# Performance work log

Hardware: AMD Instinct MI355X
Metric: run time of the kernel (lower is better)

Reference implementation:

```python
import jax, jax.numpy as jnp
import numpy as np

H, C, G = 4, 32, 64          # heads, per-head channels, num graphs
D_IN, HID = 128, 128          # input feature dim, dueling MLP hidden
NEG_SLOPE = 0.2               # GATv2Conv default negative_slope


def setup_inputs() -> dict:
    key = jax.random.key(0)
    ks = jax.random.split(key, 16)
    N, E = 50000, 800000
    x = jax.random.normal(ks[0], (N, D_IN), jnp.float32)
    edge_index = jax.random.randint(ks[1], (2, E), 0, N, dtype=jnp.int64)
    batch = jnp.sort(jax.random.randint(ks[2], (N,), 0, G, dtype=jnp.int64))
    s_in = 1.0 / np.sqrt(D_IN)
    s_g = 1.0 / np.sqrt(H * C)
    s_h = 1.0 / np.sqrt(HID)
    return {
        "x": x,
        "W_l": jax.random.normal(ks[3], (D_IN, H * C), jnp.float32) * s_in,
        "b_l": jnp.zeros((H * C,), jnp.float32),
        "W_r": jax.random.normal(ks[4], (D_IN, H * C), jnp.float32) * s_in,
        "b_r": jnp.zeros((H * C,), jnp.float32),
        "att": jax.random.normal(ks[5], (H, C), jnp.float32) * (1.0 / np.sqrt(C)),
        "bias": jnp.zeros((H * C,), jnp.float32),
        "Wq1": jax.random.normal(ks[6], (H * C, HID), jnp.float32) * s_g,
        "bq1": jnp.zeros((HID,), jnp.float32),
        "Wq2": jax.random.normal(ks[7], (HID, 2), jnp.float32) * s_h,
        "bq2": jnp.zeros((2,), jnp.float32),
        "Wv1": jax.random.normal(ks[8], (H * C, HID), jnp.float32) * s_g,
        "bv1": jnp.zeros((HID,), jnp.float32),
        "Wv2": jax.random.normal(ks[9], (HID, 1), jnp.float32) * s_h,
        "bv2": jnp.zeros((1,), jnp.float32),
        "edge_index": edge_index,
        "batch": batch,
    }


def reference(x, W_l, b_l, W_r, b_r, att, bias,
              Wq1, bq1, Wq2, bq2, Wv1, bv1, Wv2, bv2,
              edge_index, batch):
    N = x.shape[0]
    # add self loops (PyG GATv2Conv default)
    loop = jnp.arange(N, dtype=edge_index.dtype)
    src = jnp.concatenate([edge_index[0], loop])  # message source j
    dst = jnp.concatenate([edge_index[1], loop])  # aggregation target i

    xl = (x @ W_l + b_l).reshape(N, H, C)  # source transform
    xr = (x @ W_r + b_r).reshape(N, H, C)  # target transform

    # per-edge GATv2 score: a^T LeakyReLU(xl_j + xr_i), shape [Et, H]
    m = jax.nn.leaky_relu(xl[src] + xr[dst], NEG_SLOPE)
    e = jnp.einsum('ehc,hc->eh', m, att)

    # segment softmax over incoming edges of each target node
    emax = jax.ops.segment_max(e, dst, num_segments=N)
    ee = jnp.exp(e - emax[dst])
    denom = jax.ops.segment_sum(ee, dst, num_segments=N)
    alpha = ee / (denom[dst] + 1e-16)  # [Et, H]

    # scatter-add weighted source features, concat heads
    out = jax.ops.segment_sum(alpha[:, :, None] * xl[src], dst, num_segments=N)
    h = jax.nn.relu(out.reshape(N, H * C) + bias)

    # global max pool per graph
    g = jax.ops.segment_max(h, batch, num_segments=G)  # [G, H*C]

    # dueling heads
    q = jax.nn.relu(g @ Wq1 + bq1) @ Wq2 + bq2  # [G, 2]
    v = jax.nn.relu(g @ Wv1 + bv1) @ Wv2 + bv2  # [G, 1]
    return q - q.mean(axis=1, keepdims=True) + v
```

## Files before the change

### kernel.cpp

```cpp
#include <hip/hip_runtime.h>
#include <hip/hip_fp16.h>

#define F   128
#define DIN 128
#define HID 128
#define NEG 0.2f
#define L2E 1.4426950408889634f
#define KNODE 8
#define CAP  64
#define BW   64
#define EPB  2048
#define NBP  800
#define PB   128

typedef _Float16 hvec2 __attribute__((ext_vector_type(2)));
typedef _Float16 half8 __attribute__((ext_vector_type(8)));
typedef float f32x4 __attribute__((ext_vector_type(4)));
union U2 { unsigned u; hvec2 v; };
union UH { _Float16 f; unsigned short u; };

template<int CTRL>
__device__ __forceinline__ float dpp_addf(float x){
    int t = __builtin_amdgcn_update_dpp(0, __float_as_int(x), CTRL, 0xF, 0xF, true);
    return x + __int_as_float(t);
}

__global__ __launch_bounds__(256) void k_fuseA(
        const float* __restrict__ Wl, const float* __restrict__ Wr,
        const float* __restrict__ att,
        const float* __restrict__ bl, const float* __restrict__ br,
        unsigned short* __restrict__ WT, unsigned* __restrict__ att_h,
        float* __restrict__ bcat, unsigned* __restrict__ g_bits, int GF,
        const int* __restrict__ ei, unsigned* __restrict__ table, int E){
    __shared__ unsigned h[NBP];
    if ((int)blockIdx.x < PB){
        const int e = blockIdx.x * 256 + threadIdx.x;
        if (e < 32768){
            const int k = e >> 8, col = e & 255;
            const float w = (col < 128) ? Wl[k * 128 + col] : Wr[k * 128 + (col - 128)];
            UH u; u.f = (_Float16)w;
            WT[col * 128 + k] = u.u;
        }
        if (e < 64){
            float2 a2 = ((const float2*)att)[e];
            U2 r; r.v = hvec2{(_Float16)(a2.x * L2E), (_Float16)(a2.y * L2E)};
            att_h[e] = r.u;
        }
        if (e < 256) bcat[e] = (e < 128) ? bl[e] : br[e - 128];
        if (e < GF) g_bits[e] = 0u;
        return;
    }
    const int blk = (int)blockIdx.x - PB;
    const int t = threadIdx.x;
    for (int b = t; b < NBP; b += 256) h[b] = 0u;
    __syncthreads();
    const int e0 = blk * EPB;
    const int e1 = (e0 + EPB < E) ? e0 + EPB : E;
    for (int e = e0 + t; e < e1; e += 256)
        atomicAdd(&h[ei[E + e] >> 6], 1u);
    __syncthreads();
    unsigned* row = table + (size_t)blk * NBP;
    for (int b = t; b < NBP; b += 256) row[b] = h[b];
}

__global__ __launch_bounds__(512) void k_scanA(unsigned* __restrict__ table,
                        unsigned* __restrict__ btot, int B){
    __shared__ unsigned lds[512];
    const int bin = blockIdx.x;
    const int t = threadIdx.x;
    unsigned v = (t < B) ? table[(size_t)t * NBP + bin] : 0u;
    lds[t] = v; __syncthreads();
    unsigned acc = v;
    for (int off = 1; off < 512; off <<= 1){
        const unsigned add = (t >= off) ? lds[t - off] : 0u; __syncthreads();
        acc += add; lds[t] = acc; __syncthreads();
    }
    if (t < B) table[(size_t)t * NBP + bin] = acc - v;
    if (t == B - 1) btot[bin] = acc;
}

__global__ __launch_bounds__(1024) void k_scanB(const unsigned* __restrict__ btot,
                        unsigned* __restrict__ bbase, int NBK){
    __shared__ unsigned lds[1024];
    const int t = threadIdx.x;
    unsigned v = (t < NBK) ? btot[t] : 0u;
    lds[t] = v; __syncthreads();
    unsigned acc = v;
    for (int off = 1; off < 1024; off <<= 1){
        const unsigned add = (t >= off) ? lds[t - off] : 0u; __syncthreads();
        acc += add; lds[t] = acc; __syncthreads();
    }
    if (t < 1024 && t < NBP) bbase[t] = (t < NBK) ? acc - v : 0u;
}

__global__ __launch_bounds__(256) void k_eplace(const int* __restrict__ ei,
                        const unsigned* __restrict__ table, const unsigned* __restrict__ bbase,
                        unsigned* __restrict__ bucket, int E){
    __shared__ unsigned curs[NBP];
    const int t = threadIdx.x;
    const unsigned* row = table + (size_t)blockIdx.x * NBP;
    for (int b = t; b < NBP; b += 256) curs[b] = row[b] + bbase[b];
    __syncthreads();
    const int e0 = blockIdx.x * EPB;
    const int e1 = (e0 + EPB < E) ? e0 + EPB : E;
    for (int e = e0 + t; e < e1; e += 256){
        const int src = ei[e];
        const int dst = ei[E + e];
        const unsigned pos = atomicAdd(&curs[dst >> 6], 1u);
        bucket[pos] = ((unsigned)src << 6) | (unsigned)(dst & 63);
    }
}

__global__ __launch_bounds__(256) void k_fuseB(
        const unsigned* __restrict__ bbase, const unsigned* __restrict__ btot,
        const unsigned* __restrict__ bucket, unsigned* __restrict__ cnt,
        int* __restrict__ slots, int N, int NBK,
        const float* __restrict__ x, const unsigned short* __restrict__ WT,
        const float* __restrict__ bcat,
        unsigned short* __restrict__ xl_s, unsigned short* __restrict__ xr_s){
    __shared__ unsigned lc[BW];
    if ((int)blockIdx.x < NBK){
        const int b = blockIdx.x;
        const int t = threadIdx.x;
        if (t < BW) lc[t] = 0u;
        __syncthreads();
        const int base = b << 6;
        const unsigned s0 = bbase[b];
        const int n = (int)btot[b];
        for (int e = t; e < n; e += 256){
            const unsigned w = bucket[s0 + e];
            const int d = (int)(w & 63u);
            const unsigned pos = atomicAdd(&lc[d], 1u);
            if (pos < CAP - 1) slots[((size_t)(base + d) << 6) + 1 + pos] = (int)(w >> 6);
        }
        __syncthreads();
        if (t < BW && base + t < N) cnt[base + t] = lc[t];
        return;
    }
    const int mb = (int)blockIdx.x - NBK;
    const int t = threadIdx.x;
    const int w = t >> 6, lane = t & 63;
    const int li = lane & 15, hi = lane >> 4;
    const int rowA = mb * 64 + w * 16 + li;
    const int rA = (rowA < N) ? rowA : N - 1;
    f32x4 acc[16];
    #pragma unroll
    for (int c = 0; c < 16; ++c) acc[c] = f32x4{0.f, 0.f, 0.f, 0.f};
    #pragma unroll
    for (int kt = 0; kt < 4; ++kt){
        const int k0 = kt * 32 + hi * 8;
        const float4 f0 = *(const float4*)(x + (size_t)rA * DIN + k0);
        const float4 f1 = *(const float4*)(x + (size_t)rA * DIN + k0 + 4);
        half8 b;
        b[0] = (_Float16)f0.x; b[1] = (_Float16)f0.y; b[2] = (_Float16)f0.z; b[3] = (_Float16)f0.w;
        b[4] = (_Float16)f1.x; b[5] = (_Float16)f1.y; b[6] = (_Float16)f1.z; b[7] = (_Float16)f1.w;
        #pragma unroll
        for (int c = 0; c < 16; ++c){
            const half8 a = *(const half8*)(WT + (size_t)(c * 16 + li) * 128 + k0);
            acc[c] = __builtin_amdgcn_mfma_f32_16x16x32_f16(a, b, acc[c], 0, 0, 0);
        }
    }
    if (rowA < N){
        #pragma unroll
        for (int c = 0; c < 16; ++c){
            const int col0 = c * 16 + hi * 4;
            const float4 bv = *(const float4*)(bcat + col0);
            UH p0, p1, p2, p3;
            p0.f = (_Float16)(acc[c][0] + bv.x);
            p1.f = (_Float16)(acc[c][1] + bv.y);
            p2.f = (_Float16)(acc[c][2] + bv.z);
            p3.f = (_Float16)(acc[c][3] + bv.w);
            uint2 val;
            val.x = (unsigned)p0.u | ((unsigned)p1.u << 16);
            val.y = (unsigned)p2.u | ((unsigned)p3.u << 16);
            if (col0 < 128) *(uint2*)(xl_s + (size_t)rowA * F + col0)         = val;
            else            *(uint2*)(xr_s + (size_t)rowA * F + (col0 - 128)) = val;
        }
    }
}

__global__ void k_node(const unsigned* __restrict__ xl_h, const unsigned* __restrict__ xr_h,
                       const int* __restrict__ slots, const unsigned* __restrict__ cnt,
                       const unsigned* __restrict__ att_h, const float* __restrict__ bias,
                       const int* __restrict__ batch, unsigned* __restrict__ g_bits, int N){
    const int wid  = (int)(((long long)blockIdx.x * blockDim.x + threadIdx.x) >> 6);
    const int lane = threadIdx.x & 63;
    const int i0 = wid * KNODE;
    if (i0 >= N) return;
    U2 atv; atv.u = att_h[lane];
    const float2 bz = ((const float2*)bias)[lane];
    const hvec2 neg2 = {(_Float16)NEG, (_Float16)NEG};
    float pool0 = 0.f, pool1 = 0.f;
    int curg = __builtin_amdgcn_readfirstlane(batch[i0]);
    const int iend = (i0 + KNODE < N) ? i0 + KNODE : N;

    for (int i = i0; i < iend; ++i){
        const int g = __builtin_amdgcn_readfirstlane(batch[i]);
        if (g != curg){
            atomicMax(&g_bits[curg * F + 2 * lane],     __float_as_uint(pool0));
            atomicMax(&g_bits[curg * F + 2 * lane + 1], __float_as_uint(pool1));
            pool0 = 0.f; pool1 = 0.f; curg = g;
        }
        const int rs = i << 6;
        int dt = (int)cnt[i] + 1;
        if (dt > CAP) dt = CAP;
        U2 xrv; xrv.u = xr_h[(size_t)i * 64 + lane];

        float d0=0.f,d1=0.f,d2=0.f,d3=0.f,d4=0.f,d5=0.f,d6=0.f,d7=0.f;
        float ax0=0.f,ax1=0.f,ax2=0.f,ax3=0.f,ax4=0.f,ax5=0.f,ax6=0.f,ax7=0.f;
        float ay0=0.f,ay1=0.f,ay2=0.f,ay3=0.f,ay4=0.f,ay5=0.f,ay6=0.f,ay7=0.f;

        auto proc = [&](unsigned hv, float& d_, float& ax_, float& ay_){
            U2 xlv; xlv.u = hv;
            hvec2 z = xlv.v + xrv.v;
            hvec2 r = __builtin_elementwise_max(z, z * neg2);
#if __has_builtin(__builtin_amdgcn_fdot2)
            float s = __builtin_amdgcn_fdot2(r, atv.v, 0.f, false);
#else
            float s = fmaf((float)r.x, (float)atv.v.x, (float)r.y * (float)atv.v.y);
#endif
            s = dpp_addf<0xB1>(s);
            s = dpp_addf<0x4E>(s);
            s = dpp_addf<0x124>(s);
            s = dpp_addf<0x128>(s);
            const float p = exp2f(s);
            d_ += p;
            ax_ = fmaf(p, (float)xlv.v.x, ax_);
            ay_ = fmaf(p, (float)xlv.v.y, ay_);
        };

        const int my_src = (lane > 0 && lane < dt) ? slots[rs + lane] : i;
        int e = 0;
        for (; e + 7 < dt; e += 8){
            const int s0 = __builtin_amdgcn_readlane(my_src, e);
            const int s1 = __builtin_amdgcn_readlane(my_src, e + 1);
            const int s2 = __builtin_amdgcn_readlane(my_src, e + 2);
            const int s3 = __builtin_amdgcn_readlane(my_src, e + 3);
            const int s4 = __builtin_amdgcn_readlane(my_src, e + 4);
            const int s5 = __builtin_amdgcn_readlane(my_src, e + 5);
            const int s6 = __builtin_amdgcn_readlane(my_src, e + 6);
            const int s7 = __builtin_amdgcn_readlane(my_src, e + 7);
            const unsigned h0 = xl_h[(size_t)s0 * 64 + lane];
            const unsigned h1 = xl_h[(size_t)s1 * 64 + lane];
            const unsigned h2 = xl_h[(size_t)s2 * 64 + lane];
            const unsigned h3 = xl_h[(size_t)s3 * 64 + lane];
            const unsigned h4 = xl_h[(size_t)s4 * 64 + lane];
            const unsigned h5 = xl_h[(size_t)s5 * 64 + lane];
            const unsigned h6 = xl_h[(size_t)s6 * 64 + lane];
            const unsigned h7 = xl_h[(size_t)s7 * 64 + lane];
            proc(h0, d0, ax0, ay0); proc(h1, d1, ax1, ay1);
            proc(h2, d2, ax2, ay2); proc(h3, d3, ax3, ay3);
            proc(h4, d4, ax4, ay4); proc(h5, d5, ax5, ay5);
            proc(h6, d6, ax6, ay6); proc(h7, d7, ax7, ay7);
        }
        for (; e + 3 < dt; e += 4){
            const int s0 = __builtin_amdgcn_readlane(my_src, e);
            const int s1 = __builtin_amdgcn_readlane(my_src, e + 1);
            const int s2 = __builtin_amdgcn_readlane(my_src, e + 2);
            const int s3 = __builtin_amdgcn_readlane(my_src, e + 3);
            const unsigned h0 = xl_h[(size_t)s0 * 64 + lane];
            const unsigned h1 = xl_h[(size_t)s1 * 64 + lane];
            const unsigned h2 = xl_h[(size_t)s2 * 64 + lane];
            const unsigned h3 = xl_h[(size_t)s3 * 64 + lane];
            proc(h0, d0, ax0, ay0); proc(h1, d1, ax1, ay1);
            proc(h2, d2, ax2, ay2); proc(h3, d3, ax3, ay3);
        }
        for (; e < dt; ++e){
            const int s0 = __builtin_amdgcn_readlane(my_src, e);
            proc(xl_h[(size_t)s0 * 64 + lane], d0, ax0, ay0);
        }

        const float dsum = ((d0 + d1) + (d2 + d3)) + ((d4 + d5) + (d6 + d7));
        const float ax = ((ax0 + ax1) + (ax2 + ax3)) + ((ax4 + ax5) + (ax6 + ax7));
        const float ay = ((ay0 + ay1) + (ay2 + ay3)) + ((ay4 + ay5) + (ay6 + ay7));
        const float inv = 1.f / (dsum + 1e-16f);
        pool0 = fmaxf(pool0, fmaxf(fmaf(ax, inv, bz.x), 0.f));
        pool1 = fmaxf(pool1, fmaxf(fmaf(ay, inv, bz.y), 0.f));
    }
    atomicMax(&g_bits[curg * F + 2 * lane],     __float_as_uint(pool0));
    atomicMax(&g_bits[curg * F + 2 * lane + 1], __float_as_uint(pool1));
}

__global__ void k_dueling(const float* __restrict__ g,
                          const float* __restrict__ Wq1, const float* __restrict__ bq1,
                          const float* __restrict__ Wq2, const float* __restrict__ bq2,
                          const float* __restrict__ Wv1, const float* __restrict__ bv1,
                          const float* __restrict__ Wv2, const float* __restrict__ bv2,
                          float* __restrict__ out){
    __shared__ float gs[F], red0[128], red1[128], red2[128];
    const int t = threadIdx.x, gi = blockIdx.x;
    gs[t] = g[gi * F + t];
    __syncthreads();
    float aq = bq1[t], av = bv1[t];
    for (int k = 0; k < F; ++k){
        aq = fmaf(gs[k], Wq1[k * HID + t], aq);
        av = fmaf(gs[k], Wv1[k * HID + t], av);
    }
    aq = aq > 0.f ? aq : 0.f;
    av = av > 0.f ? av : 0.f;
    red0[t] = aq * Wq2[t * 2 + 0];
    red1[t] = aq * Wq2[t * 2 + 1];
    red2[t] = av * Wv2[t];
    __syncthreads();
    for (int off = 64; off > 0; off >>= 1){
        if (t < off){ red0[t] += red0[t + off]; red1[t] += red1[t + off]; red2[t] += red2[t + off]; }
        __syncthreads();
    }
    if (t == 0){
        const float q0 = red0[0] + bq2[0];
        const float q1 = red1[0] + bq2[1];
        const float v  = red2[0] + bv2[0];
        out[gi * 2 + 0] = 0.5f * (q0 - q1) + v;
        out[gi * 2 + 1] = 0.5f * (q1 - q0) + v;
    }
}

extern "C" void kernel_launch(void* const* d_in, const int* in_sizes, int n_in,
                              void* d_out, int out_size, void* d_ws, size_t ws_size,
                              hipStream_t stream) {
    const float* x    = (const float*)d_in[0];
    const float* Wl   = (const float*)d_in[1];
    const float* bl   = (const float*)d_in[2];
    const float* Wr   = (const float*)d_in[3];
    const float* br   = (const float*)d_in[4];
    const float* att  = (const float*)d_in[5];
    const float* bias = (const float*)d_in[6];
    const float* Wq1  = (const float*)d_in[7];
    const float* bq1  = (const float*)d_in[8];
    const float* Wq2  = (const float*)d_in[9];
    const float* bq2  = (const float*)d_in[10];
    const float* Wv1  = (const float*)d_in[11];
    const float* bv1  = (const float*)d_in[12];
    const float* Wv2  = (const float*)d_in[13];
    const float* bv2  = (const float*)d_in[14];
    const int*   ei   = (const int*)d_in[15];
    const int*   batch= (const int*)d_in[16];
    float* out = (float*)d_out;

    const int N  = in_sizes[0] / DIN;
    const int E  = in_sizes[15] / 2;
    const int Gg = out_size / 2;
    const int GF = Gg * F;
    const int NBK = (N + BW - 1) / BW;
    const int B   = (E + EPB - 1) / EPB;
    const int MMB = (N + 63) / 64;

    unsigned* xl_h   = (unsigned*)d_ws;
    unsigned* xr_h   = xl_h + (size_t)N * 64;
    unsigned* att_h  = xr_h + (size_t)N * 64;
    unsigned* WT     = att_h + 64;
    float*    bcat   = (float*)(WT + 16384);
    unsigned* g_bits = (unsigned*)(bcat + 256);
    unsigned* cnt    = g_bits + GF;
    unsigned* bbase  = cnt + N;
    unsigned* btot   = bbase + NBP;
    unsigned* table  = btot + NBP;
    unsigned* bucket = table + (size_t)B * NBP;
    int*      slots  = (int*)(bucket + E);

    k_fuseA<<<PB + B, 256, 0, stream>>>(Wl, Wr, att, bl, br, (unsigned short*)WT,
                                        att_h, bcat, g_bits, GF, ei, table, E);
    k_scanA<<<NBK, 512, 0, stream>>>(table, btot, B);
    k_scanB<<<1, 1024, 0, stream>>>(btot, bbase, NBK);
    k_eplace<<<B, 256, 0, stream>>>(ei, table, bbase, bucket, E);
    k_fuseB<<<NBK + MMB, 256, 0, stream>>>(bbase, btot, bucket, cnt, slots, N, NBK,
                                           x, (const unsigned short*)WT, bcat,
                                           (unsigned short*)xl_h, (unsigned short*)xr_h);
    {
        const long long waves = (N + KNODE - 1) / KNODE;
        const long long thr = waves * 64;
        k_node<<<(unsigned)((thr + 255) / 256), 256, 0, stream>>>(
            xl_h, xr_h, slots, cnt, att_h, bias, batch, g_bits, N);
    }
    k_dueling<<<Gg, 128, 0, stream>>>((const float*)g_bits, Wq1, bq1, Wq2, bq2,
                                      Wv1, bv1, Wv2, bv2, out);
}
```

Baseline: 144.8 us.

## Process two edges per wavefront step using half-waves with 4 channels per lane

The node kernel now splits each 64-lane wavefront into two 32-lane halves. Each half handles a different incoming edge, and each lane loads 4 fp16 channels (uint2) instead of 2. The per-head score reduction uses two DPP steps plus a ds_swizzle xor-4 in place of four DPP row ops. The halves are combined with a shfl_xor at the end, and only the first half does the pool atomics. This aims to halve the serial edge iterations and issue wider gathers, at the cost of shuffles for source indices, an extra cross-half reduction, and masking of odd tails.

Measured after the change: 157.4 us. +8.7%, slower.

```diff
diff --git a/kernel.cpp b/kernel.cpp
--- a/kernel.cpp
+++ b/kernel.cpp
@@ -22,6 +22,10 @@
 template<int CTRL>
 __device__ __forceinline__ float dpp_addf(float x){
     int t = __builtin_amdgcn_update_dpp(0, __float_as_int(x), CTRL, 0xF, 0xF, true);
+    return x + __int_as_float(t);
+}
+__device__ __forceinline__ float swz_xor4(float x){
+    int t = __builtin_amdgcn_ds_swizzle(__float_as_int(x), 0x101F);
     return x + __int_as_float(t);
 }
 
@@ -185,100 +189,104 @@
                        const int* __restrict__ batch, unsigned* __restrict__ g_bits, int N){
     const int wid  = (int)(((long long)blockIdx.x * blockDim.x + threadIdx.x) >> 6);
     const int lane = threadIdx.x & 63;
+    const int half = lane >> 5;
+    const int cl   = lane & 31;
     const int i0 = wid * KNODE;
     if (i0 >= N) return;
-    U2 atv; atv.u = att_h[lane];
-    const float2 bz = ((const float2*)bias)[lane];
+    const uint2 at2 = ((const uint2*)att_h)[cl];
+    U2 at0, at1; at0.u = at2.x; at1.u = at2.y;
+    const float4 bz = ((const float4*)bias)[cl];
     const hvec2 neg2 = {(_Float16)NEG, (_Float16)NEG};
-    float pool0 = 0.f, pool1 = 0.f;
+    float pool0 = 0.f, pool1 = 0.f, pool2 = 0.f, pool3 = 0.f;
     int curg = __builtin_amdgcn_readfirstlane(batch[i0]);
     const int iend = (i0 + KNODE < N) ? i0 + KNODE : N;
+    const uint2* xl2 = (const uint2*)xl_h;
 
     for (int i = i0; i < iend; ++i){
         const int g = __builtin_amdgcn_readfirstlane(batch[i]);
         if (g != curg){
-            atomicMax(&g_bits[curg * F + 2 * lane],     __float_as_uint(pool0));
-            atomicMax(&g_bits[curg * F + 2 * lane + 1], __float_as_uint(pool1));
-            pool0 = 0.f; pool1 = 0.f; curg = g;
+            if (half == 0){
+                unsigned* gb = &g_bits[curg * F + 4 * cl];
+                atomicMax(&gb[0], __float_as_uint(pool0));
+                atomicMax(&gb[1], __float_as_uint(pool1));
+                atomicMax(&gb[2], __float_as_uint(pool2));
+                atomicMax(&gb[3], __float_as_uint(pool3));
+            }
+            pool0 = pool1 = pool2 = pool3 = 0.f; curg = g;
         }
         const int rs = i << 6;
         int dt = (int)cnt[i] + 1;
         if (dt > CAP) dt = CAP;
-        U2 xrv; xrv.u = xr_h[(size_t)i * 64 + lane];
-
-        float d0=0.f,d1=0.f,d2=0.f,d3=0.f,d4=0.f,d5=0.f,d6=0.f,d7=0.f;
-        float ax0=0.f,ax1=0.f,ax2=0.f,ax3=0.f,ax4=0.f,ax5=0.f,ax6=0.f,ax7=0.f;
-        float ay0=0.f,ay1=0.f,ay2=0.f,ay3=0.f,ay4=0.f,ay5=0.f,ay6=0.f,ay7=0.f;
-
-        auto proc = [&](unsigned hv, float& d_, float& ax_, float& ay_){
-            U2 xlv; xlv.u = hv;
-            hvec2 z = xlv.v + xrv.v;
-            hvec2 r = __builtin_elementwise_max(z, z * neg2);
+        const uint2 xr2 = ((const uint2*)xr_h)[(size_t)i * 32 + cl];
+        U2 xr0, xr1; xr0.u = xr2.x; xr1.u = xr2.y;
+
+        float d0=0.f,d1=0.f,d2=0.f,d3=0.f;
+        float a00=0.f,a01=0.f,a02=0.f,a03=0.f;
+        float a10=0.f,a11=0.f,a12=0.f,a13=0.f;
+        float a20=0.f,a21=0.f,a22=0.f,a23=0.f;
+        float a30=0.f,a31=0.f,a32=0.f,a33=0.f;
+
+        const int my_src = (lane > 0 && lane < dt) ? slots[rs + lane] : i;
+
+        auto proc2 = [&](int e, float& d_, float& x0, float& x1, float& x2, float& x3){
+            const int srcv = __shfl(my_src, e + half, 64);
+            const uint2 xlv = xl2[(size_t)srcv * 32 + cl];
+            U2 b0, b1; b0.u = xlv.x; b1.u = xlv.y;
+            hvec2 z0 = b0.v + xr0.v;
+            hvec2 z1 = b1.v + xr1.v;
+            hvec2 r0 = __builtin_elementwise_max(z0, z0 * neg2);
+            hvec2 r1 = __builtin_elementwise_max(z1, z1 * neg2);
 #if __has_builtin(__builtin_amdgcn_fdot2)
-            float s = __builtin_amdgcn_fdot2(r, atv.v, 0.f, false);
+            float s = __builtin_amdgcn_fdot2(r0, at0.v, 0.f, false);
+            s = __builtin_amdgcn_fdot2(r1, at1.v, s, false);
 #else
-            float s = fmaf((float)r.x, (float)atv.v.x, (float)r.y * (float)atv.v.y);
+            float s = (float)r0.x * (float)at0.v.x + (float)r0.y * (float)at0.v.y
+                    + (float)r1.x * (float)at1.v.x + (float)r1.y * (float)at1.v.y;
 #endif
             s = dpp_addf<0xB1>(s);
             s = dpp_addf<0x4E>(s);
-            s = dpp_addf<0x124>(s);
-            s = dpp_addf<0x128>(s);
-            const float p = exp2f(s);
+            s = swz_xor4(s);
+            const float p = (e + half < dt) ? exp2f(s) : 0.f;
             d_ += p;
-            ax_ = fmaf(p, (float)xlv.v.x, ax_);
-            ay_ = fmaf(p, (float)xlv.v.y, ay_);
+            x0 = fmaf(p, (float)b0.v.x, x0);
+            x1 = fmaf(p, (float)b0.v.y, x1);
+            x2 = fmaf(p, (float)b1.v.x, x2);
+            x3 = fmaf(p, (float)b1.v.y, x3);
         };
 
-        const int my_src = (lane > 0 && lane < dt) ? slots[rs + lane] : i;
         int e = 0;
         for (; e + 7 < dt; e += 8){
-            const int s0 = __builtin_amdgcn_readlane(my_src, e);
-            const int s1 = __builtin_amdgcn_readlane(my_src, e + 1);
-            const int s2 = __builtin_amdgcn_readlane(my_src, e + 2);
-            const int s3 = __builtin_amdgcn_readlane(my_src, e + 3);
-            const int s4 = __builtin_amdgcn_readlane(my_src, e + 4);
-            const int s5 = __builtin_amdgcn_readlane(my_src, e + 5);
-            const int s6 = __builtin_amdgcn_readlane(my_src, e + 6);
-            const int s7 = __builtin_amdgcn_readlane(my_src, e + 7);
-            const unsigned h0 = xl_h[(size_t)s0 * 64 + lane];
-            const unsigned h1 = xl_h[(size_t)s1 * 64 + lane];
-            const unsigned h2 = xl_h[(size_t)s2 * 64 + lane];
-            const unsigned h3 = xl_h[(size_t)s3 * 64 + lane];
-            const unsigned h4 = xl_h[(size_t)s4 * 64 + lane];
-            const unsigned h5 = xl_h[(size_t)s5 * 64 + lane];
-            const unsigned h6 = xl_h[(size_t)s6 * 64 + lane];
-            const unsigned h7 = xl_h[(size_t)s7 * 64 + lane];
-            proc(h0, d0, ax0, ay0); proc(h1, d1, ax1, ay1);
-            proc(h2, d2, ax2, ay2); proc(h3, d3, ax3, ay3);
-            proc(h4, d4, ax4, ay4); proc(h5, d5, ax5, ay5);
-            proc(h6, d6, ax6, ay6); proc(h7, d7, ax7, ay7);
-        }
-        for (; e + 3 < dt; e += 4){
-            const int s0 = __builtin_amdgcn_readlane(my_src, e);
-            const int s1 = __builtin_amdgcn_readlane(my_src, e + 1);
-            const int s2 = __builtin_amdgcn_readlane(my_src, e + 2);
-            const int s3 = __builtin_amdgcn_readlane(my_src, e + 3);
-            const unsigned h0 = xl_h[(size_t)s0 * 64 + lane];
-            const unsigned h1 = xl_h[(size_t)s1 * 64 + lane];
-            const unsigned h2 = xl_h[(size_t)s2 * 64 + lane];
-            const unsigned h3 = xl_h[(size_t)s3 * 64 + lane];
-            proc(h0, d0, ax0, ay0); proc(h1, d1, ax1, ay1);
-            proc(h2, d2, ax2, ay2); proc(h3, d3, ax3, ay3);
-        }
-        for (; e < dt; ++e){
-            const int s0 = __builtin_amdgcn_readlane(my_src, e);
-            proc(xl_h[(size_t)s0 * 64 + lane], d0, ax0, ay0);
-        }
-
-        const float dsum = ((d0 + d1) + (d2 + d3)) + ((d4 + d5) + (d6 + d7));
-        const float ax = ((ax0 + ax1) + (ax2 + ax3)) + ((ax4 + ax5) + (ax6 + ax7));
-        const float ay = ((ay0 + ay1) + (ay2 + ay3)) + ((ay4 + ay5) + (ay6 + ay7));
-        const float inv = 1.f / (dsum + 1e-16f);
-        pool0 = fmaxf(pool0, fmaxf(fmaf(ax, inv, bz.x), 0.f));
-        pool1 = fmaxf(pool1, fmaxf(fmaf(ay, inv, bz.y), 0.f));
-    }
-    atomicMax(&g_bits[curg * F + 2 * lane],     __float_as_uint(pool0));
-    atomicMax(&g_bits[curg * F + 2 * lane + 1], __float_as_uint(pool1));
+            proc2(e,     d0, a00, a01, a02, a03);
+            proc2(e + 2, d1, a10, a11, a12, a13);
+            proc2(e + 4, d2, a20, a21, a22, a23);
+            proc2(e + 6, d3, a30, a31, a32, a33);
+        }
+        for (; e < dt; e += 2)
+            proc2(e, d0, a00, a01, a02, a03);
+
+        float d = (d0 + d1) + (d2 + d3);
+        float c0 = (a00 + a10) + (a20 + a30);
+        float c1 = (a01 + a11) + (a21 + a31);
+        float c2 = (a02 + a12) + (a22 + a32);
+        float c3 = (a03 + a13) + (a23 + a33);
+        d  += __shfl_xor(d, 32, 64);
+        c0 += __shfl_xor(c0, 32, 64);
+        c1 += __shfl_xor(c1, 32, 64);
+        c2 += __shfl_xor(c2, 32, 64);
+        c3 += __shfl_xor(c3, 32, 64);
+        const float inv = 1.f / (d + 1e-16f);
+        pool0 = fmaxf(pool0, fmaxf(fmaf(c0, inv, bz.x), 0.f));
+        pool1 = fmaxf(pool1, fmaxf(fmaf(c1, inv, bz.y), 0.f));
+        pool2 = fmaxf(pool2, fmaxf(fmaf(c2, inv, bz.z), 0.f));
+        pool3 = fmaxf(pool3, fmaxf(fmaf(c3, inv, bz.w), 0.f));
+    }
+    if (half == 0){
+        unsigned* gb = &g_bits[curg * F + 4 * cl];
+        atomicMax(&gb[0], __float_as_uint(pool0));
+        atomicMax(&gb[1], __float_as_uint(pool1));
+        atomicMax(&gb[2], __float_as_uint(pool2));
+        atomicMax(&gb[3], __float_as_uint(pool3));
+    }
 }
 
 __global__ void k_dueling(const float* __restrict__ g,
```
